# Kernel tuning notes

Hardware: AMD Instinct MI355X
Metric: run time of the kernel (lower is better)

Reference implementation:

```python
import jax, jax.numpy as jnp
import numpy as np
from jax import lax

T, B, I, N, C, L = 512, 256, 64, 512, 10, 3
TAU = 2.0  # train_tau=False -> constant, non-trainable


def setup_inputs() -> dict:
    key = jax.random.key(0)
    ks = jax.random.split(key, 12)
    f32 = jnp.float32
    data = jax.random.normal(ks[0], (T, B, I), f32)
    h0 = 0.1 * jax.random.uniform(ks[1], (L, B, N), f32)  # matches 0.1*torch.rand init
    # Linear params; weights stored as [in, out] so y = x @ W + b
    Win = jax.random.normal(ks[2], (I, N), f32) / np.float32(np.sqrt(I))
    b_in = 0.01 * jax.random.normal(ks[3], (N,), f32)
    Whh = jax.random.normal(ks[4], (L, N, N), f32) / np.float32(np.sqrt(N))
    b_hh = 0.01 * jax.random.normal(ks[5], (L, N), f32)
    Whi = jax.random.normal(ks[6], (L - 1, N, N), f32) / np.float32(np.sqrt(N))
    b_hi = 0.01 * jax.random.normal(ks[7], (L - 1, N), f32)
    Wfc = jax.random.normal(ks[8], (N, C), f32) / np.float32(np.sqrt(N))
    b_fc = 0.01 * jax.random.normal(ks[9], (C,), f32)
    return {"data": data, "h0": h0, "Win": Win, "b_in": b_in,
            "Whh": Whh, "b_hh": b_hh, "Whi": Whi, "b_hi": b_hi,
            "Wfc": Wfc, "b_fc": b_fc}


def reference(data, h0, Win, b_in, Whh, b_hh, Whi, b_hi, Wfc, b_fc):
    alpha = 1.0 - 1.0 / TAU
    # forward() zeroes the recurrent diagonal every call
    Whh = Whh * (1.0 - jnp.eye(N, dtype=Whh.dtype))
    x = data @ Win + b_in  # [T, B, N] input projection (single input layer, mean over 1)

    def step(hs, inp):
        h0_, h1_, h2_ = hs
        # layer 0: leaky integration + LeakyReLU; same inp fed to every layer
        n0 = jax.nn.leaky_relu(alpha * h0_ + (h0_ @ Whh[0] + b_hh[0] + inp) / TAU)
        # layer 1 sees the *updated* layer-0 state (sequential within a timestep)
        n1 = jax.nn.leaky_relu(
            alpha * h1_ + (h1_ @ Whh[1] + b_hh[1] + n0 @ Whi[0] + b_hi[0] + inp) / TAU)
        n2 = jax.nn.leaky_relu(
            alpha * h2_ + (h2_ @ Whh[2] + b_hh[2] + n1 @ Whi[1] + b_hi[1] + inp) / TAU)
        return (n0, n1, n2), None

    hs_final, _ = lax.scan(step, (h0[0], h0[1], h0[2]), x)
    out = hs_final[-1] @ Wfc + b_fc  # [B, C], single readout head
    return out
```

## Files before the change

### kernel.cpp

```cpp
#include <hip/hip_runtime.h>
#include <stdint.h>


#define TS    512
#define BB    256
#define NN    512
#define MR    16
#define NRG   16
#define NCT   4
#define RD    8
#define LROW  520

typedef __attribute__((ext_vector_type(8))) short s8v;
typedef __attribute__((ext_vector_type(4))) float f4v;
typedef __attribute__((ext_vector_type(4))) unsigned int u4v;

#define MFMA16(a, b, c) __builtin_amdgcn_mfma_f32_16x16x32_bf16((a), (b), (c), 0, 0, 0)

__device__ __forceinline__ short f2bf(float f) {
  union { float f; unsigned u; } v; v.f = f;
  unsigned u = v.u;
  u += 0x7fffu + ((u >> 16) & 1u);
  return (short)(u >> 16);
}

__device__ __forceinline__ s8v pack8(f4v a, f4v b) {
  s8v v;
  v[0] = f2bf(a[0]); v[1] = f2bf(a[1]); v[2] = f2bf(a[2]); v[3] = f2bf(a[3]);
  v[4] = f2bf(b[0]); v[5] = f2bf(b[1]); v[6] = f2bf(b[2]); v[7] = f2bf(b[3]);
  return v;
}

__device__ __forceinline__ u4v ldg_sc1_x4(const unsigned short* p) {
  u4v r;
  asm volatile("global_load_dwordx4 %0, %1, off sc1" : "=v"(r) : "v"(p));
  return r;
}
__device__ __forceinline__ void stg_sc1_b16(unsigned short* p, unsigned v) {
  asm volatile("global_store_short %0, %1, off sc1" :: "v"(p), "v"(v) : "memory");
}
__device__ __forceinline__ void waitvm0() {
  asm volatile("s_waitcnt vmcnt(0)" ::: "memory");
}

__global__ __launch_bounds__(256, 1) void rnn_pipe(
    const float* __restrict__ data, const float* __restrict__ h0,
    const float* __restrict__ Win,  const float* __restrict__ b_in,
    const float* __restrict__ Whh,  const float* __restrict__ b_hh,
    const float* __restrict__ Whi,  const float* __restrict__ b_hi,
    unsigned short* __restrict__ ring, unsigned* __restrict__ cnt,
    float* __restrict__ hfinal)
{
  __shared__ __attribute__((aligned(16))) unsigned short qtile[MR * LROW];
  __shared__ __attribute__((aligned(16))) unsigned short ptile[MR * LROW];

  const int bi   = blockIdx.x;
  const int lay  = bi % 3;
  const int rest = bi / 3;
  const int rg   = rest & 15;
  const int ct   = rest >> 4;
  const int tid  = threadIdx.x;
  const int wv   = tid >> 6;
  const int lane = tid & 63;
  const int lo   = lane & 15;
  const int q4   = lane >> 4;
  const int row0 = rg * MR;
  const int cw   = ct * 128 + wv * 32;

  const int sidx = (lay * NRG + rg) * NCT + ct;
  unsigned* selfprod = cnt + (size_t)sidx * 32;
  unsigned* selfdone = cnt + (size_t)(256 + sidx) * 32;

  unsigned* pollptr = selfprod;
  int polltype = 0;
  if (lane < 4) {
    pollptr = cnt + (size_t)((lay * NRG + rg) * NCT + lane) * 32;  polltype = 1;
  } else if (lane >= 4 && lane < 8 && lay > 0) {
    pollptr = cnt + (size_t)(((lay - 1) * NRG + rg) * NCT + (lane - 4)) * 32;  polltype = 2;
  } else if (lane >= 8 && lane < 12 && lay < 2) {
    pollptr = cnt + (size_t)(256 + ((lay + 1) * NRG + rg) * NCT + (lane - 8)) * 32;  polltype = 3;
  }

  s8v WH[16][2];
  s8v WI[16][2];
  s8v WX[2][2];
  float biasv[2];
  f4v  hst[2];

  {
    const float* WmH = Whh + (size_t)lay * NN * NN;
    #pragma unroll
    for (int kk = 0; kk < 16; ++kk) {
      #pragma unroll
      for (int nf = 0; nf < 2; ++nf) {
        const int col = cw + nf * 16 + lo;
        s8v v;
        #pragma unroll
        for (int j = 0; j < 8; ++j) {
          const int k = kk * 32 + q4 * 8 + j;
          float f = WmH[(size_t)k * NN + col];
          if (k == col) f = 0.f;
          v[j] = f2bf(f);
        }
        WH[kk][nf] = v;
      }
    }
    if (lay > 0) {
      const float* WmI = Whi + (size_t)(lay - 1) * NN * NN;
      #pragma unroll
      for (int kk = 0; kk < 16; ++kk) {
        #pragma unroll
        for (int nf = 0; nf < 2; ++nf) {
          const int col = cw + nf * 16 + lo;
          s8v v;
          #pragma unroll
          for (int j = 0; j < 8; ++j)
            v[j] = f2bf(WmI[(size_t)(kk * 32 + q4 * 8 + j) * NN + col]);
          WI[kk][nf] = v;
        }
      }
    }
    #pragma unroll
    for (int kk = 0; kk < 2; ++kk) {
      #pragma unroll
      for (int nf = 0; nf < 2; ++nf) {
        const int col = cw + nf * 16 + lo;
        s8v v;
        #pragma unroll
        for (int j = 0; j < 8; ++j)
          v[j] = f2bf(Win[(size_t)(kk * 32 + q4 * 8 + j) * NN + col]);
        WX[kk][nf] = v;
      }
    }
    #pragma unroll
    for (int nf = 0; nf < 2; ++nf) {
      const int col = cw + nf * 16 + lo;
      float b = b_hh[lay * NN + col] + b_in[col];
      if (lay > 0) b += b_hi[(lay - 1) * NN + col];
      biasv[nf] = b;
      #pragma unroll
      for (int r = 0; r < 4; ++r)
        hst[nf][r] = h0[(size_t)lay * BB * NN + (size_t)(row0 + q4 * 4 + r) * NN + col];
    }
  }

  const size_t myring = (size_t)(lay * NRG + rg) * RD;
  const size_t upring = (size_t)((lay - 1) * NRG + rg) * RD;

  for (int t = 0; t < TS; ++t) {
    unsigned tgt = 0;
    if (polltype == 1) tgt = (unsigned)t;
    else if (polltype == 2) tgt = (unsigned)(t + 1);
    else if (polltype == 3 && t >= RD) tgt = (unsigned)(t - RD + 1);
    for (;;) {
      unsigned v = __hip_atomic_load(pollptr, __ATOMIC_RELAXED, __HIP_MEMORY_SCOPE_AGENT);
      if (__all(v >= tgt)) break;
    }

    u4v qst[4], pst[4];
    if (t >= 1) {
      const unsigned short* src = ring + (myring + ((t - 1) & (RD - 1))) * (MR * NN);
      #pragma unroll
      for (int i = 0; i < 4; ++i) {
        const int chunk = i * 256 + tid;
        qst[i] = ldg_sc1_x4(src + (chunk >> 6) * NN + (chunk & 63) * 8);
      }
    }
    if (lay > 0) {
      const unsigned short* src = ring + (upring + (t & (RD - 1))) * (MR * NN);
      #pragma unroll
      for (int i = 0; i < 4; ++i) {
        const int chunk = i * 256 + tid;
        pst[i] = ldg_sc1_x4(src + (chunk >> 6) * NN + (chunk & 63) * 8);
      }
    }
    waitvm0();
    if (t >= 1) {
      #pragma unroll
      for (int i = 0; i < 4; ++i) {
        const int chunk = i * 256 + tid;
        *(u4v*)(qtile + (chunk >> 6) * LROW + (chunk & 63) * 8) = qst[i];
      }
    }
    if (lay > 0) {
      #pragma unroll
      for (int i = 0; i < 4; ++i) {
        const int chunk = i * 256 + tid;
        *(u4v*)(ptile + (chunk >> 6) * LROW + (chunk & 63) * 8) = pst[i];
      }
    }
    __syncthreads();
    if (tid == 0 && lay > 0)
      __hip_atomic_store(selfdone, (unsigned)(t + 1), __ATOMIC_RELAXED,
                         __HIP_MEMORY_SCOPE_AGENT);

    f4v zero4 = {0.f, 0.f, 0.f, 0.f};
    f4v acc[2] = {zero4, zero4};

    {
      const float* dsrc = data + ((size_t)t * BB + row0 + lo) * 64 + q4 * 8;
      #pragma unroll
      for (int kk = 0; kk < 2; ++kk) {
        f4v a = *(const f4v*)(dsrc + kk * 32);
        f4v b = *(const f4v*)(dsrc + kk * 32 + 4);
        s8v av = pack8(a, b);
        acc[0] = MFMA16(av, WX[kk][0], acc[0]);
        acc[1] = MFMA16(av, WX[kk][1], acc[1]);
      }
    }
    if (lay > 0) {
      #pragma unroll
      for (int kk = 0; kk < 16; ++kk) {
        s8v av = *(const s8v*)(ptile + lo * LROW + kk * 32 + q4 * 8);
        acc[0] = MFMA16(av, WI[kk][0], acc[0]);
        acc[1] = MFMA16(av, WI[kk][1], acc[1]);
      }
    }
    if (t == 0) {
      const float* hsrc = h0 + (size_t)lay * BB * NN + (size_t)(row0 + lo) * NN + q4 * 8;
      #pragma unroll
      for (int kk = 0; kk < 16; ++kk) {
        f4v a = *(const f4v*)(hsrc + kk * 32);
        f4v b = *(const f4v*)(hsrc + kk * 32 + 4);
        s8v av = pack8(a, b);
        acc[0] = MFMA16(av, WH[kk][0], acc[0]);
        acc[1] = MFMA16(av, WH[kk][1], acc[1]);
      }
    } else {
      #pragma unroll
      for (int kk = 0; kk < 16; ++kk) {
        s8v av = *(const s8v*)(qtile + lo * LROW + kk * 32 + q4 * 8);
        acc[0] = MFMA16(av, WH[kk][0], acc[0]);
        acc[1] = MFMA16(av, WH[kk][1], acc[1]);
      }
    }

    {
      unsigned short* rslot = ring + (myring + (t & (RD - 1))) * (MR * NN);
      #pragma unroll
      for (int nf = 0; nf < 2; ++nf) {
        const int col = cw + nf * 16 + lo;
        #pragma unroll
        for (int r = 0; r < 4; ++r) {
          const int row = q4 * 4 + r;
          float v = 0.5f * hst[nf][r] + 0.5f * (acc[nf][r] + biasv[nf]);
          v = (v >= 0.f) ? v : 0.01f * v;
          hst[nf][r] = v;
          stg_sc1_b16(rslot + (size_t)row * NN + col,
                      (unsigned)(unsigned short)f2bf(v));
          if (lay == 2 && t == TS - 1)
            hfinal[(size_t)(row0 + row) * NN + col] = v;
        }
      }
    }
    waitvm0();
    __syncthreads();
    if (tid == 0)
      __hip_atomic_store(selfprod, (unsigned)(t + 1), __ATOMIC_RELAXED,
                         __HIP_MEMORY_SCOPE_AGENT);
  }
}

__global__ void readout_k(const float* __restrict__ hfinal, const float* __restrict__ Wfc,
                          const float* __restrict__ b_fc, float* __restrict__ out)
{
  const int row = blockIdx.x;
  const int lane = threadIdx.x;
  float a[10];
  #pragma unroll
  for (int c = 0; c < 10; ++c) a[c] = 0.f;
  for (int k = lane; k < NN; k += 64) {
    const float h = hfinal[(size_t)row * NN + k];
    const float* w = Wfc + (size_t)k * 10;
    #pragma unroll
    for (int c = 0; c < 10; ++c) a[c] += h * w[c];
  }
  #pragma unroll
  for (int off = 32; off > 0; off >>= 1) {
    #pragma unroll
    for (int c = 0; c < 10; ++c) a[c] += __shfl_down(a[c], off);
  }
  if (lane == 0) {
    #pragma unroll
    for (int c = 0; c < 10; ++c) out[row * 10 + c] = a[c] + b_fc[c];
  }
}

extern "C" void kernel_launch(void* const* d_in, const int* in_sizes, int n_in,
                              void* d_out, int out_size, void* d_ws, size_t ws_size,
                              hipStream_t stream) {
  (void)in_sizes; (void)n_in; (void)out_size; (void)ws_size;
  const float* data = (const float*)d_in[0];
  const float* h0   = (const float*)d_in[1];
  const float* Win  = (const float*)d_in[2];
  const float* b_in = (const float*)d_in[3];
  const float* Whh  = (const float*)d_in[4];
  const float* b_hh = (const float*)d_in[5];
  const float* Whi  = (const float*)d_in[6];
  const float* b_hi = (const float*)d_in[7];
  const float* Wfc  = (const float*)d_in[8];
  const float* b_fc = (const float*)d_in[9];

  unsigned short* ring = (unsigned short*)d_ws;
  const size_t ring_bytes = (size_t)3 * NRG * RD * MR * NN * 2;
  unsigned* cnt = (unsigned*)((char*)d_ws + ring_bytes);
  float* hfinal = (float*)((char*)d_ws + ring_bytes + 65536);

  hipMemsetAsync(cnt, 0, 65536, stream);
  hipLaunchKernelGGL(rnn_pipe, dim3(192), dim3(256), 0, stream,
                     data, h0, Win, b_in, Whh, b_hh, Whi, b_hi, ring, cnt, hfinal);
  hipLaunchKernelGGL(readout_k, dim3(256), dim3(64), 0, stream,
                     hfinal, Wfc, b_fc, (float*)d_out);
}
```

Measured before the change: 2.381 ms.

## Replace block barriers and LDS staging with per-wave flags and direct ring loads

Each wave now loads its MFMA A-operands straight from the global ring buffer into registers, replacing the cooperative LDS staging and the __syncthreads barriers. Progress counters become per-wave (16 per row group) instead of per-block, so consumers poll 16 flags each and producers signal as soon as their own wave finishes. The input projection load is hoisted before the poll loop, an s_sleep is added to the spin, and the recurrent and inter-layer products go into separate accumulators. This removes block-wide barriers from the per-timestep critical path, at the cost of redundant global reads (every wave reads the full 16x512 tiles) and more flag traffic.

```diff
diff --git a/kernel.cpp b/kernel.cpp
--- a/kernel.cpp
+++ b/kernel.cpp
@@ -9,11 +9,9 @@
 #define NRG   16
 #define NCT   4
 #define RD    8
-#define LROW  520
 
 typedef __attribute__((ext_vector_type(8))) short s8v;
 typedef __attribute__((ext_vector_type(4))) float f4v;
-typedef __attribute__((ext_vector_type(4))) unsigned int u4v;
 
 #define MFMA16(a, b, c) __builtin_amdgcn_mfma_f32_16x16x32_bf16((a), (b), (c), 0, 0, 0)
 
@@ -31,11 +29,33 @@
   return v;
 }
 
-__device__ __forceinline__ u4v ldg_sc1_x4(const unsigned short* p) {
-  u4v r;
-  asm volatile("global_load_dwordx4 %0, %1, off sc1" : "=v"(r) : "v"(p));
-  return r;
-}
+__device__ __forceinline__ void ld16_sync(s8v o[16], const unsigned short* p) {
+  asm volatile(
+      "global_load_dwordx4 %0,  %16, off sc1\n\t"
+      "global_load_dwordx4 %1,  %16, off offset:64 sc1\n\t"
+      "global_load_dwordx4 %2,  %16, off offset:128 sc1\n\t"
+      "global_load_dwordx4 %3,  %16, off offset:192 sc1\n\t"
+      "global_load_dwordx4 %4,  %16, off offset:256 sc1\n\t"
+      "global_load_dwordx4 %5,  %16, off offset:320 sc1\n\t"
+      "global_load_dwordx4 %6,  %16, off offset:384 sc1\n\t"
+      "global_load_dwordx4 %7,  %16, off offset:448 sc1\n\t"
+      "global_load_dwordx4 %8,  %16, off offset:512 sc1\n\t"
+      "global_load_dwordx4 %9,  %16, off offset:576 sc1\n\t"
+      "global_load_dwordx4 %10, %16, off offset:640 sc1\n\t"
+      "global_load_dwordx4 %11, %16, off offset:704 sc1\n\t"
+      "global_load_dwordx4 %12, %16, off offset:768 sc1\n\t"
+      "global_load_dwordx4 %13, %16, off offset:832 sc1\n\t"
+      "global_load_dwordx4 %14, %16, off offset:896 sc1\n\t"
+      "global_load_dwordx4 %15, %16, off offset:960 sc1\n\t"
+      "s_waitcnt vmcnt(0)"
+      : "=&v"(o[0]), "=&v"(o[1]), "=&v"(o[2]), "=&v"(o[3]),
+        "=&v"(o[4]), "=&v"(o[5]), "=&v"(o[6]), "=&v"(o[7]),
+        "=&v"(o[8]), "=&v"(o[9]), "=&v"(o[10]), "=&v"(o[11]),
+        "=&v"(o[12]), "=&v"(o[13]), "=&v"(o[14]), "=&v"(o[15])
+      : "v"(p)
+      : "memory");
+}
+
 __device__ __forceinline__ void stg_sc1_b16(unsigned short* p, unsigned v) {
   asm volatile("global_store_short %0, %1, off sc1" :: "v"(p), "v"(v) : "memory");
 }
@@ -51,9 +71,6 @@
     unsigned short* __restrict__ ring, unsigned* __restrict__ cnt,
     float* __restrict__ hfinal)
 {
-  __shared__ __attribute__((aligned(16))) unsigned short qtile[MR * LROW];
-  __shared__ __attribute__((aligned(16))) unsigned short ptile[MR * LROW];
-
   const int bi   = blockIdx.x;
   const int lay  = bi % 3;
   const int rest = bi / 3;
@@ -66,19 +83,20 @@
   const int q4   = lane >> 4;
   const int row0 = rg * MR;
   const int cw   = ct * 128 + wv * 32;
-
-  const int sidx = (lay * NRG + rg) * NCT + ct;
-  unsigned* selfprod = cnt + (size_t)sidx * 32;
-  unsigned* selfdone = cnt + (size_t)(256 + sidx) * 32;
-
-  unsigned* pollptr = selfprod;
+  const int wci  = ct * 4 + wv;
+
+  const int fq = (lay * NRG + rg) * 16;
+  unsigned* myprod = cnt + (size_t)(fq + wci) * 32;
+  unsigned* mydone = cnt + (size_t)(768 + fq + wci) * 32;
+
+  unsigned* pollptr = myprod;
   int polltype = 0;
-  if (lane < 4) {
-    pollptr = cnt + (size_t)((lay * NRG + rg) * NCT + lane) * 32;  polltype = 1;
-  } else if (lane >= 4 && lane < 8 && lay > 0) {
-    pollptr = cnt + (size_t)(((lay - 1) * NRG + rg) * NCT + (lane - 4)) * 32;  polltype = 2;
-  } else if (lane >= 8 && lane < 12 && lay < 2) {
-    pollptr = cnt + (size_t)(256 + ((lay + 1) * NRG + rg) * NCT + (lane - 8)) * 32;  polltype = 3;
+  if (lane < 16) {
+    pollptr = cnt + (size_t)(fq + lane) * 32;  polltype = 1;
+  } else if (lane < 32 && lay > 0) {
+    pollptr = cnt + (size_t)(((lay - 1) * NRG + rg) * 16 + (lane - 16)) * 32;  polltype = 2;
+  } else if (lane >= 32 && lane < 48 && lay < 2) {
+    pollptr = cnt + (size_t)(768 + ((lay + 1) * NRG + rg) * 16 + (lane - 32)) * 32;  polltype = 3;
   }
 
   s8v WH[16][2];
@@ -148,90 +166,68 @@
   const size_t upring = (size_t)((lay - 1) * NRG + rg) * RD;
 
   for (int t = 0; t < TS; ++t) {
+    const float* dsrc = data + ((size_t)t * BB + row0 + lo) * 64 + q4 * 8;
+    f4v xa0 = *(const f4v*)(dsrc + 0);
+    f4v xa1 = *(const f4v*)(dsrc + 4);
+    f4v xa2 = *(const f4v*)(dsrc + 32);
+    f4v xa3 = *(const f4v*)(dsrc + 36);
+
     unsigned tgt = 0;
     if (polltype == 1) tgt = (unsigned)t;
     else if (polltype == 2) tgt = (unsigned)(t + 1);
     else if (polltype == 3 && t >= RD) tgt = (unsigned)(t - RD + 1);
     for (;;) {
       unsigned v = __hip_atomic_load(pollptr, __ATOMIC_RELAXED, __HIP_MEMORY_SCOPE_AGENT);
-      if (__all(v >= tgt)) break;
-    }
-
-    u4v qst[4], pst[4];
+      if (__all((int)(v >= tgt))) break;
+      __builtin_amdgcn_s_sleep(1);
+    }
+
+    f4v zero4 = {0.f, 0.f, 0.f, 0.f};
+    f4v accQ[2] = {zero4, zero4};
+    f4v accP[2] = {zero4, zero4};
+    {
+      s8v xv0 = pack8(xa0, xa1);
+      s8v xv1 = pack8(xa2, xa3);
+      accQ[0] = MFMA16(xv0, WX[0][0], accQ[0]);
+      accQ[1] = MFMA16(xv0, WX[0][1], accQ[1]);
+      accQ[0] = MFMA16(xv1, WX[1][0], accQ[0]);
+      accQ[1] = MFMA16(xv1, WX[1][1], accQ[1]);
+    }
+
     if (t >= 1) {
-      const unsigned short* src = ring + (myring + ((t - 1) & (RD - 1))) * (MR * NN);
-      #pragma unroll
-      for (int i = 0; i < 4; ++i) {
-        const int chunk = i * 256 + tid;
-        qst[i] = ldg_sc1_x4(src + (chunk >> 6) * NN + (chunk & 63) * 8);
-      }
-    }
-    if (lay > 0) {
-      const unsigned short* src = ring + (upring + (t & (RD - 1))) * (MR * NN);
-      #pragma unroll
-      for (int i = 0; i < 4; ++i) {
-        const int chunk = i * 256 + tid;
-        pst[i] = ldg_sc1_x4(src + (chunk >> 6) * NN + (chunk & 63) * 8);
-      }
-    }
-    waitvm0();
-    if (t >= 1) {
-      #pragma unroll
-      for (int i = 0; i < 4; ++i) {
-        const int chunk = i * 256 + tid;
-        *(u4v*)(qtile + (chunk >> 6) * LROW + (chunk & 63) * 8) = qst[i];
-      }
-    }
-    if (lay > 0) {
-      #pragma unroll
-      for (int i = 0; i < 4; ++i) {
-        const int chunk = i * 256 + tid;
-        *(u4v*)(ptile + (chunk >> 6) * LROW + (chunk & 63) * 8) = pst[i];
-      }
-    }
-    __syncthreads();
-    if (tid == 0 && lay > 0)
-      __hip_atomic_store(selfdone, (unsigned)(t + 1), __ATOMIC_RELAXED,
-                         __HIP_MEMORY_SCOPE_AGENT);
-
-    f4v zero4 = {0.f, 0.f, 0.f, 0.f};
-    f4v acc[2] = {zero4, zero4};
-
-    {
-      const float* dsrc = data + ((size_t)t * BB + row0 + lo) * 64 + q4 * 8;
-      #pragma unroll
-      for (int kk = 0; kk < 2; ++kk) {
-        f4v a = *(const f4v*)(dsrc + kk * 32);
-        f4v b = *(const f4v*)(dsrc + kk * 32 + 4);
-        s8v av = pack8(a, b);
-        acc[0] = MFMA16(av, WX[kk][0], acc[0]);
-        acc[1] = MFMA16(av, WX[kk][1], acc[1]);
-      }
-    }
-    if (lay > 0) {
+      s8v qa[16];
+      const unsigned short* qsrc =
+          ring + (myring + ((t - 1) & (RD - 1))) * (MR * NN) + (size_t)lo * NN + q4 * 8;
+      ld16_sync(qa, qsrc);
       #pragma unroll
       for (int kk = 0; kk < 16; ++kk) {
-        s8v av = *(const s8v*)(ptile + lo * LROW + kk * 32 + q4 * 8);
-        acc[0] = MFMA16(av, WI[kk][0], acc[0]);
-        acc[1] = MFMA16(av, WI[kk][1], acc[1]);
-      }
-    }
-    if (t == 0) {
+        accQ[0] = MFMA16(qa[kk], WH[kk][0], accQ[0]);
+        accQ[1] = MFMA16(qa[kk], WH[kk][1], accQ[1]);
+      }
+    } else {
       const float* hsrc = h0 + (size_t)lay * BB * NN + (size_t)(row0 + lo) * NN + q4 * 8;
       #pragma unroll
       for (int kk = 0; kk < 16; ++kk) {
         f4v a = *(const f4v*)(hsrc + kk * 32);
         f4v b = *(const f4v*)(hsrc + kk * 32 + 4);
         s8v av = pack8(a, b);
-        acc[0] = MFMA16(av, WH[kk][0], acc[0]);
-        acc[1] = MFMA16(av, WH[kk][1], acc[1]);
-      }
-    } else {
+        accQ[0] = MFMA16(av, WH[kk][0], accQ[0]);
+        accQ[1] = MFMA16(av, WH[kk][1], accQ[1]);
+      }
+    }
+
+    if (lay > 0) {
+      s8v pa[16];
+      const unsigned short* psrc =
+          ring + (upring + (t & (RD - 1))) * (MR * NN) + (size_t)lo * NN + q4 * 8;
+      ld16_sync(pa, psrc);
+      if (lane == 0)
+        __hip_atomic_store(mydone, (unsigned)(t + 1), __ATOMIC_RELAXED,
+                           __HIP_MEMORY_SCOPE_AGENT);
       #pragma unroll
       for (int kk = 0; kk < 16; ++kk) {
-        s8v av = *(const s8v*)(qtile + lo * LROW + kk * 32 + q4 * 8);
-        acc[0] = MFMA16(av, WH[kk][0], acc[0]);
-        acc[1] = MFMA16(av, WH[kk][1], acc[1]);
+        accP[0] = MFMA16(pa[kk], WI[kk][0], accP[0]);
+        accP[1] = MFMA16(pa[kk], WI[kk][1], accP[1]);
       }
     }
 
@@ -243,7 +239,7 @@
         #pragma unroll
         for (int r = 0; r < 4; ++r) {
           const int row = q4 * 4 + r;
-          float v = 0.5f * hst[nf][r] + 0.5f * (acc[nf][r] + biasv[nf]);
+          float v = 0.5f * hst[nf][r] + 0.5f * (accQ[nf][r] + accP[nf][r] + biasv[nf]);
           v = (v >= 0.f) ? v : 0.01f * v;
           hst[nf][r] = v;
           stg_sc1_b16(rslot + (size_t)row * NN + col,
@@ -254,9 +250,8 @@
       }
     }
     waitvm0();
-    __syncthreads();
-    if (tid == 0)
-      __hip_atomic_store(selfprod, (unsigned)(t + 1), __ATOMIC_RELAXED,
+    if (lane == 0)
+      __hip_atomic_store(myprod, (unsigned)(t + 1), __ATOMIC_RELAXED,
                          __HIP_MEMORY_SCOPE_AGENT);
   }
 }
@@ -304,9 +299,9 @@
   unsigned short* ring = (unsigned short*)d_ws;
   const size_t ring_bytes = (size_t)3 * NRG * RD * MR * NN * 2;
   unsigned* cnt = (unsigned*)((char*)d_ws + ring_bytes);
-  float* hfinal = (float*)((char*)d_ws + ring_bytes + 65536);
-
-  hipMemsetAsync(cnt, 0, 65536, stream);
+  float* hfinal = (float*)((char*)d_ws + ring_bytes + 262144);
+
+  hipMemsetAsync(cnt, 0, 262144, stream);
   hipLaunchKernelGGL(rnn_pipe, dim3(192), dim3(256), 0, stream,
                      data, h0, Win, b_in, Whh, b_hh, Whi, b_hi, ring, cnt, hfinal);
   hipLaunchKernelGGL(readout_k, dim3(256), dim3(64), 0, stream,
```

Result: slower. 3.335 ms (+40.1%).

## Prefetch input rows and hoist input MFMA ahead of ring poll

Applied to the files above, without the earlier changes.

The next timestep's input data is now loaded at the end of each step, and the input-projection MFMAs run before the spin-wait on the producer counter, so their latency overlaps the wait. Ring loads are merged into one inline-asm block with per-thread contiguous 64-byte chunks and immediate offsets, issuing all q and p loads before a single wait. The chunk-to-thread mapping changes, which alters the global and LDS access patterns and may add LDS bank conflicts or poorer coalescing. Register pressure also rises from the held prefetch values.

```diff
diff --git a/kernel.cpp b/kernel.cpp
--- a/kernel.cpp
+++ b/kernel.cpp
@@ -31,11 +31,35 @@
   return v;
 }
 
-__device__ __forceinline__ u4v ldg_sc1_x4(const unsigned short* p) {
-  u4v r;
-  asm volatile("global_load_dwordx4 %0, %1, off sc1" : "=v"(r) : "v"(p));
-  return r;
-}
+__device__ __forceinline__ void ld8_sync(u4v o[8], const unsigned short* qp,
+                                         const unsigned short* pp) {
+  asm volatile(
+      "global_load_dwordx4 %0, %8, off sc1\n\t"
+      "global_load_dwordx4 %1, %8, off offset:16 sc1\n\t"
+      "global_load_dwordx4 %2, %8, off offset:32 sc1\n\t"
+      "global_load_dwordx4 %3, %8, off offset:48 sc1\n\t"
+      "global_load_dwordx4 %4, %9, off sc1\n\t"
+      "global_load_dwordx4 %5, %9, off offset:16 sc1\n\t"
+      "global_load_dwordx4 %6, %9, off offset:32 sc1\n\t"
+      "global_load_dwordx4 %7, %9, off offset:48 sc1\n\t"
+      "s_waitcnt vmcnt(0)"
+      : "=&v"(o[0]), "=&v"(o[1]), "=&v"(o[2]), "=&v"(o[3]),
+        "=&v"(o[4]), "=&v"(o[5]), "=&v"(o[6]), "=&v"(o[7])
+      : "v"(qp), "v"(pp)
+      : "memory");
+}
+__device__ __forceinline__ void ld4_sync(u4v o[4], const unsigned short* p) {
+  asm volatile(
+      "global_load_dwordx4 %0, %4, off sc1\n\t"
+      "global_load_dwordx4 %1, %4, off offset:16 sc1\n\t"
+      "global_load_dwordx4 %2, %4, off offset:32 sc1\n\t"
+      "global_load_dwordx4 %3, %4, off offset:48 sc1\n\t"
+      "s_waitcnt vmcnt(0)"
+      : "=&v"(o[0]), "=&v"(o[1]), "=&v"(o[2]), "=&v"(o[3])
+      : "v"(p)
+      : "memory");
+}
+
 __device__ __forceinline__ void stg_sc1_b16(unsigned short* p, unsigned v) {
   asm volatile("global_store_short %0, %1, off sc1" :: "v"(p), "v"(v) : "memory");
 }
@@ -147,46 +171,64 @@
   const size_t myring = (size_t)(lay * NRG + rg) * RD;
   const size_t upring = (size_t)((lay - 1) * NRG + rg) * RD;
 
+  f4v xa0, xa1, xa2, xa3;
+  {
+    const float* dsrc = data + ((size_t)0 * BB + row0 + lo) * 64 + q4 * 8;
+    xa0 = *(const f4v*)(dsrc + 0);
+    xa1 = *(const f4v*)(dsrc + 4);
+    xa2 = *(const f4v*)(dsrc + 32);
+    xa3 = *(const f4v*)(dsrc + 36);
+  }
+
   for (int t = 0; t < TS; ++t) {
+    f4v zero4 = {0.f, 0.f, 0.f, 0.f};
+    f4v acc[2] = {zero4, zero4};
+    {
+      s8v xv0 = pack8(xa0, xa1);
+      s8v xv1 = pack8(xa2, xa3);
+      acc[0] = MFMA16(xv0, WX[0][0], acc[0]);
+      acc[1] = MFMA16(xv0, WX[0][1], acc[1]);
+      acc[0] = MFMA16(xv1, WX[1][0], acc[0]);
+      acc[1] = MFMA16(xv1, WX[1][1], acc[1]);
+    }
+
     unsigned tgt = 0;
     if (polltype == 1) tgt = (unsigned)t;
     else if (polltype == 2) tgt = (unsigned)(t + 1);
     else if (polltype == 3 && t >= RD) tgt = (unsigned)(t - RD + 1);
     for (;;) {
       unsigned v = __hip_atomic_load(pollptr, __ATOMIC_RELAXED, __HIP_MEMORY_SCOPE_AGENT);
-      if (__all(v >= tgt)) break;
-    }
-
-    u4v qst[4], pst[4];
-    if (t >= 1) {
-      const unsigned short* src = ring + (myring + ((t - 1) & (RD - 1))) * (MR * NN);
-      #pragma unroll
-      for (int i = 0; i < 4; ++i) {
-        const int chunk = i * 256 + tid;
-        qst[i] = ldg_sc1_x4(src + (chunk >> 6) * NN + (chunk & 63) * 8);
-      }
-    }
-    if (lay > 0) {
-      const unsigned short* src = ring + (upring + (t & (RD - 1))) * (MR * NN);
-      #pragma unroll
-      for (int i = 0; i < 4; ++i) {
-        const int chunk = i * 256 + tid;
-        pst[i] = ldg_sc1_x4(src + (chunk >> 6) * NN + (chunk & 63) * 8);
-      }
-    }
-    waitvm0();
-    if (t >= 1) {
-      #pragma unroll
-      for (int i = 0; i < 4; ++i) {
-        const int chunk = i * 256 + tid;
-        *(u4v*)(qtile + (chunk >> 6) * LROW + (chunk & 63) * 8) = qst[i];
-      }
-    }
-    if (lay > 0) {
-      #pragma unroll
-      for (int i = 0; i < 4; ++i) {
-        const int chunk = i * 256 + tid;
-        *(u4v*)(ptile + (chunk >> 6) * LROW + (chunk & 63) * 8) = pst[i];
+      if (__all((int)(v >= tgt))) break;
+    }
+
+    {
+      const unsigned short* qsrc =
+          ring + (myring + ((t - 1) & (RD - 1))) * (MR * NN) + (size_t)tid * 32;
+      const unsigned short* psrc =
+          ring + (upring + (t & (RD - 1))) * (MR * NN) + (size_t)tid * 32;
+      u4v st[8];
+      if (t >= 1 && lay > 0) {
+        ld8_sync(st, qsrc, psrc);
+        #pragma unroll
+        for (int i = 0; i < 4; ++i) {
+          const int c = tid * 4 + i;
+          *(u4v*)(qtile + (c >> 6) * LROW + (c & 63) * 8) = st[i];
+          *(u4v*)(ptile + (c >> 6) * LROW + (c & 63) * 8) = st[4 + i];
+        }
+      } else if (t >= 1) {
+        ld4_sync(st, qsrc);
+        #pragma unroll
+        for (int i = 0; i < 4; ++i) {
+          const int c = tid * 4 + i;
+          *(u4v*)(qtile + (c >> 6) * LROW + (c & 63) * 8) = st[i];
+        }
+      } else if (lay > 0) {
+        ld4_sync(st, psrc);
+        #pragma unroll
+        for (int i = 0; i < 4; ++i) {
+          const int c = tid * 4 + i;
+          *(u4v*)(ptile + (c >> 6) * LROW + (c & 63) * 8) = st[i];
+        }
       }
     }
     __syncthreads();
@@ -194,20 +236,6 @@
       __hip_atomic_store(selfdone, (unsigned)(t + 1), __ATOMIC_RELAXED,
                          __HIP_MEMORY_SCOPE_AGENT);
 
-    f4v zero4 = {0.f, 0.f, 0.f, 0.f};
-    f4v acc[2] = {zero4, zero4};
-
-    {
-      const float* dsrc = data + ((size_t)t * BB + row0 + lo) * 64 + q4 * 8;
-      #pragma unroll
-      for (int kk = 0; kk < 2; ++kk) {
-        f4v a = *(const f4v*)(dsrc + kk * 32);
-        f4v b = *(const f4v*)(dsrc + kk * 32 + 4);
-        s8v av = pack8(a, b);
-        acc[0] = MFMA16(av, WX[kk][0], acc[0]);
-        acc[1] = MFMA16(av, WX[kk][1], acc[1]);
-      }
-    }
     if (lay > 0) {
       #pragma unroll
       for (int kk = 0; kk < 16; ++kk) {
@@ -252,6 +280,15 @@
             hfinal[(size_t)(row0 + row) * NN + col] = v;
         }
       }
+    }
+
+    {
+      const int tn = (t + 1 < TS) ? t + 1 : t;
+      const float* dsrc = data + ((size_t)tn * BB + row0 + lo) * 64 + q4 * 8;
+      xa0 = *(const f4v*)(dsrc + 0);
+      xa1 = *(const f4v*)(dsrc + 4);
+      xa2 = *(const f4v*)(dsrc + 32);
+      xa3 = *(const f4v*)(dsrc + 36);
     }
     waitvm0();
     __syncthreads();
```

Result: no change. 2.339 ms (-1.8%).
